# Optimization experiments

Measured on AMD Instinct MI355X. Metric: run time of the kernel, lower is better.

Reference implementation:

```python
import jax, jax.numpy as jnp
import numpy as np
from jax import lax

EPS = 1e-20
_A, _B, _C = slice(None, -2), slice(1, -1), slice(2, None)
# 4 direction pairs: (up-left, down-right), (up, down), (up-right, down-left), (right, left)
_OFFS = [((_A, _A), (_C, _C)), ((_A, _B), (_C, _B)), ((_A, _C), (_C, _A)), ((_B, _C), (_B, _A))]


def _neigh(x, pad_val):
    # x: [B,C,H,W] -> [B,C,9,H,W] of 3x3 neighborhoods (stride 1, pad 1)
    B, C, H, W = x.shape
    xp = jnp.pad(x, ((0, 0), (0, 0), (1, 1), (1, 1)), constant_values=pad_val)
    return jnp.stack([xp[:, :, i:i + H, j:j + W] for i in range(3) for j in range(3)], axis=2)


def _take(n, j):
    return jnp.take_along_axis(n, j, axis=2)[:, :, 0]


def _pair_stack(lo, hi, op):
    # -> [B,C,2,4,H,W]; mirrors the torch stack-of-stacks over 4 directions x 2 orderings
    return jnp.stack([jnp.stack([op(lo[:, :, r1, c1], hi[:, :, r2, c2]),
                                 op(hi[:, :, r1, c1], lo[:, :, r2, c2])], axis=2)
                      for (r1, c1), (r2, c2) in _OFFS], axis=3)


def _forward(d, cd, e, ce, w_prop, w_s_from_d, channel_weight, spatial_weight):
    B, C, H, W = d.shape
    O4 = spatial_weight.shape[0]
    O = O4 // 4
    # pad like F.pad(d, (1,1,1,1))
    dp = jnp.pad(d, ((0, 0), (0, 0), (1, 1), (1, 1)))
    cdp = jnp.pad(cd, ((0, 0), (0, 0), (1, 1), (1, 1)))
    # max_pool2d(k=3,s=1,p=1, return_indices) equivalent: argmax over 3x3 neighborhood,
    # then gather d / cd at those indices (retrieve_indices)
    j_max = jnp.argmax(_neigh(dp * cdp, -np.inf), axis=2, keepdims=True)
    j_min = jnp.argmax(_neigh(cdp / (dp + EPS), -np.inf), axis=2, keepdims=True)
    nd, ncd = _neigh(dp, 0.0), _neigh(cdp, 0.0)
    d_min, d_max = _take(nd, j_min), _take(nd, j_max)
    cd_min, cd_max = _take(ncd, j_min), _take(ncd, j_max)
    # directional depth ratios and confidence products: [B,C,2,4,H,W]
    d_ratio = jnp.clip(_pair_stack(d_min, d_max, lambda a, b: a / (b + EPS)), EPS, 1.0) ** w_s_from_d
    c_ratio = _pair_stack(cd_min, cd_max, lambda a, b: a * b)
    j = jnp.argmax(c_ratio / d_ratio, axis=2, keepdims=True)
    e_from_d = _take(d_ratio, j)   # [B,C,4,H,W]
    ce_from_d = _take(c_ratio, j)  # [B,C,4,H,W]
    # confidence-weighted propagation, then flatten to [B, C*4, H, W]
    e = ((w_prop * ce * e + ce_from_d * e_from_d) / (w_prop * ce + ce_from_d + EPS)).reshape(B, C * 4, H, W)
    ce = ((w_prop * ce + ce_from_d) / (w_prop + 1.0)).reshape(B, C * 4, H, W)
    # 1x1 channel mixing conv (groups=1)
    cw = channel_weight[:, :, 0, 0]  # [O*4, C*4]
    nom = jnp.einsum('bihw,oi->bohw', ce * e, cw)
    den = jnp.einsum('bihw,oi->bohw', ce, cw)
    e = nom / (den + EPS)
    ce = den / (jnp.sum(channel_weight) + EPS)
    # depthwise spatial conv (groups = out*4), stride=1, padding=k//2
    K = spatial_weight.shape[-1]
    p = K // 2
    dw = lambda x: lax.conv_general_dilated(x, spatial_weight, (1, 1), ((p, p), (p, p)),
                                            feature_group_count=O4,
                                            dimension_numbers=('NCHW', 'OIHW', 'NCHW'))
    nom = dw(ce * e).reshape(B, O, 4, H, W)
    den = dw(ce).reshape(B, O, 4, H, W)
    return nom / (den + EPS), den / (jnp.sum(spatial_weight) + EPS)


def setup_inputs() -> dict:
    key = jax.random.key(0)
    ks = jax.random.split(key, 8)
    B, C, O, H, W, K = 4, 32, 32, 192, 192, 5
    d = jax.random.uniform(ks[0], (B, C, H, W), jnp.float32)
    cd = jax.random.uniform(ks[1], (B, C, H, W), jnp.float32)
    e = jax.random.uniform(ks[2], (B, C, 4, H, W), jnp.float32)
    ce = jax.random.uniform(ks[3], (B, C, 4, H, W), jnp.float32)
    # parameters; positive as enforced by enforce_limits() (softplus) in the original
    w_prop = jax.random.uniform(ks[4], (1, C, 1, 1, 1), jnp.float32, 0.5, 1.5)
    w_s_from_d = jax.random.uniform(ks[5], (1, C, 2, 4, 1, 1), jnp.float32, 0.5, 2.0)
    channel_weight = jax.random.uniform(ks[6], (O * 4, C * 4, 1, 1), jnp.float32)
    spatial_weight = jax.random.uniform(ks[7], (O * 4, 1, K, K), jnp.float32)
    return dict(d=d, cd=cd, e=e, ce=ce, w_prop=w_prop, w_s_from_d=w_s_from_d,
                channel_weight=channel_weight, spatial_weight=spatial_weight)


def reference(d, cd, e, ce, w_prop, w_s_from_d, channel_weight, spatial_weight):
    return _forward(d, cd, e, ce, w_prop, w_s_from_d, channel_weight, spatial_weight)
```

## Files before the change

kernel.cpp:

```cpp
#include <hip/hip_runtime.h>
#include <stdint.h>

#define EPS 1e-20f
#define H_ 192
#define W_ 192
#define HW_ 36864
#define CH4 128
#define OUTELEMS 18874368

typedef __attribute__((ext_vector_type(8))) short bf16x8;
typedef __attribute__((ext_vector_type(4))) float f32x4;

__device__ __forceinline__ unsigned short f2bf(float f) {
  unsigned u = __float_as_uint(f);
  return (unsigned short)((u + 0x7fffu + ((u >> 16) & 1u)) >> 16);
}
__device__ __forceinline__ float bflo(unsigned v) { return __uint_as_float(v << 16); }
__device__ __forceinline__ float bfhi(unsigned v) { return __uint_as_float(v & 0xffff0000u); }

__global__ void __launch_bounds__(256) k0_prep(const float* __restrict__ cw,
                                               const float* __restrict__ sw,
                                               unsigned short* __restrict__ AWhi,
                                               unsigned short* __restrict__ AWlo,
                                               float* __restrict__ sums) {
  int tid = threadIdx.x;
  if (blockIdx.x < 64) {
    int n = blockIdx.x * 256 + tid;
    int t = n & 7;
    int l = (n >> 3) & 63;
    int kb = (n >> 9) & 3;
    int ot = n >> 11;
    int o = ot * 16 + (l & 15);
    int i = kb * 32 + (l >> 4) * 8 + t;
    float wv = cw[o * 128 + i];
    unsigned short hi = f2bf(wv);
    float hif = bflo((unsigned)hi);
    unsigned short lo = f2bf(wv - hif);
    AWhi[n] = hi;
    AWlo[n] = lo;
  } else {
    __shared__ float red[256];
    float s = 0.f;
    for (int k = tid; k < 16384; k += 256) s += cw[k];
    red[tid] = s; __syncthreads();
    for (int off = 128; off > 0; off >>= 1) {
      if (tid < off) red[tid] += red[tid + off];
      __syncthreads();
    }
    if (tid == 0) sums[0] = red[0];
    __syncthreads();
    s = 0.f;
    for (int k = tid; k < 3200; k += 256) s += sw[k];
    red[tid] = s; __syncthreads();
    for (int off = 128; off > 0; off >>= 1) {
      if (tid < off) red[tid] += red[tid + off];
      __syncthreads();
    }
    if (tid == 0) sums[1] = red[0];
  }
}

__global__ void __launch_bounds__(256) k1_stage1(
    const float* __restrict__ d, const float* __restrict__ cd,
    const float* __restrict__ e, const float* __restrict__ ce,
    const float* __restrict__ wprop, const float* __restrict__ wsd,
    unsigned* __restrict__ XY) {
  const int tid = threadIdx.x;
  const int tile = blockIdx.x;
  const int th0 = (tile / 6) * 32, tw0 = (tile % 6) * 32;
  const int bc = blockIdx.y;
  const int b = bc >> 5, c = bc & 31;

  __shared__ float dpL[1296], cdpL[1296], kxL[1296], knL[1296];
  __shared__ unsigned jxn[1156];

  const float* dB = d + bc * HW_;
  const float* cdB = cd + bc * HW_;
  for (int idx = tid; idx < 1296; idx += 256) {
    int ly = idx / 36, lx = idx % 36;
    int gy = th0 + ly - 2, gx = tw0 + lx - 2;
    float dv = 0.f, cv = 0.f;
    if (gy >= 0 && gy < H_ && gx >= 0 && gx < W_) {
      dv = dB[gy * W_ + gx];
      cv = cdB[gy * W_ + gx];
    }
    dpL[idx] = dv; cdpL[idx] = cv;
    bool inb = (gy >= -1) & (gy <= H_) & (gx >= -1) & (gx <= W_);
    kxL[idx] = inb ? dv * cv : -1.f;
    knL[idx] = inb ? cv / (dv + EPS) : -1.f;
  }
  __syncthreads();

  for (int idx = tid; idx < 1156; idx += 256) {
    int ly = idx / 34, lx = idx % 34;
    int base = ly * 36 + lx;
    float bkx = -1.f, bkn = -1.f;
    int ox = base + 37, on = base + 37;
#pragma unroll
    for (int di = 0; di < 3; ++di) {
#pragma unroll
      for (int dj = 0; dj < 3; ++dj) {
        int o = base + di * 36 + dj;
        float kx = kxL[o], kn = knL[o];
        if (kx > bkx) { bkx = kx; ox = o; }
        if (kn > bkn) { bkn = kn; on = o; }
      }
    }
    jxn[idx] = (unsigned)ox | ((unsigned)on << 16);
  }
  __syncthreads();

  const float wp = wprop[c];
  const float iwp1 = __builtin_amdgcn_rcpf(wp + 1.0f);
  float wq[8];
#pragma unroll
  for (int t = 0; t < 8; ++t) wq[t] = wsd[c * 8 + t];

  const int offy[4] = {-1, -1, -1, 0};
  const int offx[4] = {-1, 0, 1, 1};

  for (int idx = tid; idx < 1024; idx += 256) {
    int ly = idx >> 5, lx = idx & 31;
    int hh = th0 + ly, ww = tw0 + lx;
#pragma unroll
    for (int p = 0; p < 4; ++p) {
      int n1 = (ly + offy[p] + 1) * 34 + (lx + offx[p] + 1);
      int n2 = (ly - offy[p] + 1) * 34 + (lx - offx[p] + 1);
      unsigned u1 = jxn[n1], u2 = jxn[n2];
      int x1i = u1 & 0xffffu, m1i = u1 >> 16;
      int x2i = u2 & 0xffffu, m2i = u2 >> 16;
      float dmn1 = dpL[m1i], cmn1 = cdpL[m1i];
      float dmx1 = dpL[x1i], cmx1 = cdpL[x1i];
      float dmn2 = dpL[m2i], cmn2 = cdpL[m2i];
      float dmx2 = dpL[x2i], cmx2 = cdpL[x2i];
      float r0 = dmn1 * __builtin_amdgcn_rcpf(dmx2 + EPS);
      float r1 = dmx1 * __builtin_amdgcn_rcpf(dmn2 + EPS);
      float cr0 = cmn1 * cmx2;
      float cr1 = cmx1 * cmn2;
      float x0 = fminf(fmaxf(r0, EPS), 1.0f);
      float x1 = fminf(fmaxf(r1, EPS), 1.0f);
      float dr0 = __builtin_amdgcn_exp2f(wq[p] * __builtin_amdgcn_logf(x0));
      float dr1 = __builtin_amdgcn_exp2f(wq[4 + p] * __builtin_amdgcn_logf(x1));
      float ef, cf;
      if (cr1 * dr0 > cr0 * dr1) { ef = dr1; cf = cr1; } else { ef = dr0; cf = cr0; }
      int ei = (bc * 4 + p) * HW_ + hh * W_ + ww;
      float ev = e[ei], cev = ce[ei];
      float dn = wp * cev + cf;
      float e1 = (wp * cev * ev + cf * ef) * __builtin_amdgcn_rcpf(dn + EPS);
      float ce1 = dn * iwp1;
      XY[(b * CH4 + c * 4 + p) * HW_ + hh * W_ + ww] =
          (unsigned)f2bf(ce1 * e1) | ((unsigned)f2bf(ce1) << 16);
    }
  }
}

__global__ void __launch_bounds__(256) k2_mix(const unsigned* __restrict__ XY,
                                              const unsigned short* __restrict__ AWhi,
                                              const unsigned short* __restrict__ AWlo,
                                              const float* __restrict__ sums,
                                              unsigned* __restrict__ PQ) {
  __shared__ unsigned L[128 * 66];
  const int tid = threadIdx.x;
  const int blk = blockIdx.x;
  const int b = blk / 576;
  const int hw0 = (blk % 576) * 64;
  const unsigned* xp = XY + (size_t)(b * CH4) * HW_ + hw0;

#pragma unroll
  for (int j = 0; j < 8; ++j) {
    int v = j * 256 + tid;
    int ch = v >> 4;
    int po = (v & 15) * 4;
    uint4 val = *reinterpret_cast<const uint4*>(xp + (size_t)ch * HW_ + po);
    unsigned* dst = &L[ch * 66 + po];
    *reinterpret_cast<uint2*>(dst) = make_uint2(val.x, val.y);
    *reinterpret_cast<uint2*>(dst + 2) = make_uint2(val.z, val.w);
  }
  __syncthreads();

  const int lane = tid & 63;
  const int w = tid >> 6;
  const int c = lane & 15;
  const int g = lane >> 4;
  const int pbase = w * 16 + c;

  bf16x8 xf[4], yf[4];
#pragma unroll
  for (int kb = 0; kb < 4; ++kb) {
    unsigned vv[8];
    const unsigned* base = &L[(kb * 32 + g * 8) * 66 + pbase];
#pragma unroll
    for (int t = 0; t < 8; ++t) vv[t] = base[t * 66];
    union { bf16x8 v; unsigned u[4]; } ux, uy;
#pragma unroll
    for (int p = 0; p < 4; ++p) {
      ux.u[p] = (vv[2 * p] & 0xffffu) | (vv[2 * p + 1] << 16);
      uy.u[p] = (vv[2 * p] >> 16) | (vv[2 * p + 1] & 0xffff0000u);
    }
    xf[kb] = ux.v;
    yf[kb] = uy.v;
  }

  const float inv = 1.0f / (sums[0] + EPS);
  unsigned* qp = PQ + (size_t)(b * CH4) * HW_ + hw0;

#pragma unroll 2
  for (int ot = 0; ot < 8; ++ot) {
    f32x4 accn = {0.f, 0.f, 0.f, 0.f};
    f32x4 accd = {0.f, 0.f, 0.f, 0.f};
#pragma unroll
    for (int kb = 0; kb < 4; ++kb) {
      int an = ((ot * 4 + kb) * 64 + lane) * 8;
      bf16x8 ahi = *reinterpret_cast<const bf16x8*>(AWhi + an);
      bf16x8 alo = *reinterpret_cast<const bf16x8*>(AWlo + an);
      accn = __builtin_amdgcn_mfma_f32_16x16x32_bf16(ahi, xf[kb], accn, 0, 0, 0);
      accn = __builtin_amdgcn_mfma_f32_16x16x32_bf16(alo, xf[kb], accn, 0, 0, 0);
      accd = __builtin_amdgcn_mfma_f32_16x16x32_bf16(ahi, yf[kb], accd, 0, 0, 0);
      accd = __builtin_amdgcn_mfma_f32_16x16x32_bf16(alo, yf[kb], accd, 0, 0, 0);
    }
#pragma unroll
    for (int j = 0; j < 4; ++j) {
      int o = ot * 16 + g * 4 + j;
      qp[(size_t)o * HW_ + w * 16 + c] =
          (unsigned)f2bf(accn[j] * inv) | ((unsigned)f2bf(accd[j] * inv) << 16);
    }
  }
}

__global__ void __launch_bounds__(256) k3_conv(const unsigned* __restrict__ PQ,
                                               const float* __restrict__ sw,
                                               const float* __restrict__ sums,
                                               float* __restrict__ out0,
                                               float* __restrict__ out1) {
  int t = blockIdx.x;
  int tile = t % 36;
  int chb = t / 36;
  int ch = chb & 127;
  int th0 = (tile / 6) * 32, tw0 = (tile % 6) * 32;
  __shared__ float Pt[1296], Qt[1296];
  const unsigned* src = PQ + chb * HW_;
  int tid = threadIdx.x;
  for (int idx = tid; idx < 1296; idx += 256) {
    int ly = idx / 36, lx = idx % 36;
    int gy = th0 + ly - 2, gx = tw0 + lx - 2;
    unsigned v = 0;
    if (gy >= 0 && gy < H_ && gx >= 0 && gx < W_) v = src[gy * W_ + gx];
    Pt[idx] = bflo(v); Qt[idx] = bfhi(v);
  }
  __syncthreads();
  float wr[25];
#pragma unroll
  for (int k = 0; k < 25; ++k) wr[k] = sw[ch * 25 + k];
  float isw = 1.0f / (sums[1] + EPS);
  int x = tid & 31, yg = tid >> 5;
  float an[4] = {0, 0, 0, 0}, ad[4] = {0, 0, 0, 0};
#pragma unroll
  for (int rr = 0; rr < 8; ++rr) {
    int Lr = yg * 4 + rr;
    float pv[5], qv[5];
#pragma unroll
    for (int c5 = 0; c5 < 5; ++c5) {
      pv[c5] = Pt[Lr * 36 + x + c5];
      qv[c5] = Qt[Lr * 36 + x + c5];
    }
#pragma unroll
    for (int k = 0; k < 4; ++k) {
      int ky = rr - k;
      if (ky >= 0 && ky <= 4) {
#pragma unroll
        for (int c5 = 0; c5 < 5; ++c5) {
          an[k] += pv[c5] * wr[ky * 5 + c5];
          ad[k] += qv[c5] * wr[ky * 5 + c5];
        }
      }
    }
  }
#pragma unroll
  for (int k = 0; k < 4; ++k) {
    int hh = th0 + yg * 4 + k;
    int oi = chb * HW_ + hh * W_ + tw0 + x;
    out0[oi] = an[k] / (ad[k] + EPS);
    out1[oi] = ad[k] * isw;
  }
}

extern "C" void kernel_launch(void* const* d_in, const int* in_sizes, int n_in,
                              void* d_out, int out_size, void* d_ws, size_t ws_size,
                              hipStream_t stream) {
  const float* d = (const float*)d_in[0];
  const float* cd = (const float*)d_in[1];
  const float* e = (const float*)d_in[2];
  const float* ce = (const float*)d_in[3];
  const float* wprop = (const float*)d_in[4];
  const float* wsd = (const float*)d_in[5];
  const float* cw = (const float*)d_in[6];
  const float* sw = (const float*)d_in[7];

  float* wsf = (float*)d_ws;
  float* sums = wsf;
  unsigned short* AWhi = (unsigned short*)(wsf + 64);
  unsigned short* AWlo = AWhi + 16384;
  unsigned* PQ = (unsigned*)(wsf + 64 + 16384);
  float* out0 = (float*)d_out;
  float* out1 = out0 + OUTELEMS;
  unsigned* XY = (unsigned*)(out0 + OUTELEMS);

  hipLaunchKernelGGL(k0_prep, dim3(65), dim3(256), 0, stream, cw, sw, AWhi, AWlo, sums);
  hipLaunchKernelGGL(k1_stage1, dim3(36, 128), dim3(256), 0, stream, d, cd, e, ce,
                     wprop, wsd, XY);
  hipLaunchKernelGGL(k2_mix, dim3(2304), dim3(256), 0, stream, XY, AWhi, AWlo, sums, PQ);
  hipLaunchKernelGGL(k3_conv, dim3(18432), dim3(256), 0, stream, PQ, sw, sums, out0,
                     out1);
}
```

Before: 417.1 us.

## Precompute gathered min/max values in shared memory and vectorize stage-1 I/O

```diff
diff --git a/kernel.cpp b/kernel.cpp
--- a/kernel.cpp
+++ b/kernel.cpp
@@ -71,8 +71,11 @@
   const int bc = blockIdx.y;
   const int b = bc >> 5, c = bc & 31;
 
-  __shared__ float dpL[1296], cdpL[1296], kxL[1296], knL[1296];
-  __shared__ unsigned jxn[1156];
+  __shared__ float S[5184];
+  float* dpL = S;
+  float* cdpL = S + 1296;
+  float* kxL = S + 2592;
+  float* knL = S + 3888;
 
   const float* dB = d + bc * HW_;
   const float* cdB = cd + bc * HW_;
@@ -91,22 +94,46 @@
   }
   __syncthreads();
 
-  for (int idx = tid; idx < 1156; idx += 256) {
-    int ly = idx / 34, lx = idx % 34;
-    int base = ly * 36 + lx;
-    float bkx = -1.f, bkn = -1.f;
-    int ox = base + 37, on = base + 37;
-#pragma unroll
-    for (int di = 0; di < 3; ++di) {
-#pragma unroll
-      for (int dj = 0; dj < 3; ++dj) {
-        int o = base + di * 36 + dj;
-        float kx = kxL[o], kn = knL[o];
-        if (kx > bkx) { bkx = kx; ox = o; }
-        if (kn > bkn) { bkn = kn; on = o; }
+  float rdmn[5], rdmx[5], rcmn[5], rcmx[5];
+#pragma unroll
+  for (int i = 0; i < 5; ++i) {
+    int idx = i * 256 + tid;
+    if (idx < 1156) {
+      int ly = idx / 34, lx = idx % 34;
+      int base = ly * 36 + lx;
+      float bkx = -1.f, bkn = -1.f;
+      int ox = base + 37, on = base + 37;
+#pragma unroll
+      for (int di = 0; di < 3; ++di) {
+#pragma unroll
+        for (int dj = 0; dj < 3; ++dj) {
+          int o = base + di * 36 + dj;
+          float kx = kxL[o], kn = knL[o];
+          if (kx > bkx) { bkx = kx; ox = o; }
+          if (kn > bkn) { bkn = kn; on = o; }
+        }
       }
-    }
-    jxn[idx] = (unsigned)ox | ((unsigned)on << 16);
+      rdmx[i] = dpL[ox]; rcmx[i] = cdpL[ox];
+      rdmn[i] = dpL[on]; rcmn[i] = cdpL[on];
+    } else {
+      rdmx[i] = 0.f; rcmx[i] = 0.f; rdmn[i] = 0.f; rcmn[i] = 0.f;
+    }
+  }
+  __syncthreads();
+
+  float* DMN = S;
+  float* DMX = S + 1190;
+  float* CMN = S + 2380;
+  float* CMX = S + 3570;
+#pragma unroll
+  for (int i = 0; i < 5; ++i) {
+    int idx = i * 256 + tid;
+    if (idx < 1156) {
+      int ly = idx / 34, lx = idx % 34;
+      int m = ly * 35 + lx;
+      DMN[m] = rdmn[i]; DMX[m] = rdmx[i];
+      CMN[m] = rcmn[i]; CMX[m] = rcmx[i];
+    }
   }
   __syncthreads();
 
@@ -119,20 +146,24 @@
   const int offy[4] = {-1, -1, -1, 0};
   const int offx[4] = {-1, 0, 1, 1};
 
-  for (int idx = tid; idx < 1024; idx += 256) {
-    int ly = idx >> 5, lx = idx & 31;
-    int hh = th0 + ly, ww = tw0 + lx;
-#pragma unroll
-    for (int p = 0; p < 4; ++p) {
-      int n1 = (ly + offy[p] + 1) * 34 + (lx + offx[p] + 1);
-      int n2 = (ly - offy[p] + 1) * 34 + (lx - offx[p] + 1);
-      unsigned u1 = jxn[n1], u2 = jxn[n2];
-      int x1i = u1 & 0xffffu, m1i = u1 >> 16;
-      int x2i = u2 & 0xffffu, m2i = u2 >> 16;
-      float dmn1 = dpL[m1i], cmn1 = cdpL[m1i];
-      float dmx1 = dpL[x1i], cmx1 = cdpL[x1i];
-      float dmn2 = dpL[m2i], cmn2 = cdpL[m2i];
-      float dmx2 = dpL[x2i], cmx2 = cdpL[x2i];
+  const int ly = tid >> 3, lx4 = (tid & 7) << 2;
+  const int hh = th0 + ly, ww0 = tw0 + lx4;
+#pragma unroll
+  for (int p = 0; p < 4; ++p) {
+    int n1 = (ly + offy[p] + 1) * 35 + (lx4 + offx[p] + 1);
+    int n2 = (ly - offy[p] + 1) * 35 + (lx4 - offx[p] + 1);
+    int ei = (bc * 4 + p) * HW_ + hh * W_ + ww0;
+    float4 ev4 = *reinterpret_cast<const float4*>(&e[ei]);
+    float4 cev4 = *reinterpret_cast<const float4*>(&ce[ei]);
+    const float* evp = &ev4.x;
+    const float* cevp = &cev4.x;
+    unsigned ow[4];
+#pragma unroll
+    for (int k = 0; k < 4; ++k) {
+      float dmn1 = DMN[n1 + k], cmn1 = CMN[n1 + k];
+      float dmx1 = DMX[n1 + k], cmx1 = CMX[n1 + k];
+      float dmn2 = DMN[n2 + k], cmn2 = CMN[n2 + k];
+      float dmx2 = DMX[n2 + k], cmx2 = CMX[n2 + k];
       float r0 = dmn1 * __builtin_amdgcn_rcpf(dmx2 + EPS);
       float r1 = dmx1 * __builtin_amdgcn_rcpf(dmn2 + EPS);
       float cr0 = cmn1 * cmx2;
@@ -143,14 +174,14 @@
       float dr1 = __builtin_amdgcn_exp2f(wq[4 + p] * __builtin_amdgcn_logf(x1));
       float ef, cf;
       if (cr1 * dr0 > cr0 * dr1) { ef = dr1; cf = cr1; } else { ef = dr0; cf = cr0; }
-      int ei = (bc * 4 + p) * HW_ + hh * W_ + ww;
-      float ev = e[ei], cev = ce[ei];
+      float ev = evp[k], cev = cevp[k];
       float dn = wp * cev + cf;
       float e1 = (wp * cev * ev + cf * ef) * __builtin_amdgcn_rcpf(dn + EPS);
       float ce1 = dn * iwp1;
-      XY[(b * CH4 + c * 4 + p) * HW_ + hh * W_ + ww] =
-          (unsigned)f2bf(ce1 * e1) | ((unsigned)f2bf(ce1) << 16);
-    }
+      ow[k] = (unsigned)f2bf(ce1 * e1) | ((unsigned)f2bf(ce1) << 16);
+    }
+    unsigned* xo = &XY[(b * CH4 + c * 4 + p) * HW_ + hh * W_ + ww0];
+    *reinterpret_cast<uint4*>(xo) = make_uint4(ow[0], ow[1], ow[2], ow[3]);
   }
 }
 
```

Result: no change. 417.5 us (+0.1%).
